# Kernel optimization log

Hardware: AMD Instinct MI355X
Metric: run time of the kernel (lower is better)

Reference implementation:

```python
import jax, jax.numpy as jnp
import numpy as np

B, L, LATENT, HID, NTOK = 65536, 8, 256, 128, 5


def setup_inputs() -> dict:
    key = jax.random.key(0)
    ks = jax.random.split(key, 8)
    s = 0.05  # small init scale for stable GRU dynamics
    return {
        "latent_context": jax.random.normal(ks[0], (B, LATENT), jnp.float32),
        "target_sequence": jax.random.randint(ks[1], (B, L), 0, NTOK),
        "emb_table": jax.random.normal(ks[2], (NTOK + 1, HID), jnp.float32) * s,
        "W_ih": jax.random.normal(ks[3], (3 * LATENT, HID), jnp.float32) * s,
        "W_hh": jax.random.normal(ks[4], (3 * LATENT, LATENT), jnp.float32) * s,
        "b_ih": jnp.zeros((3 * LATENT,), jnp.float32),
        "b_hh": jnp.zeros((3 * LATENT,), jnp.float32),
        "W_out": jax.random.normal(ks[5], (NTOK, LATENT), jnp.float32) * s,
        "b_out": jnp.zeros((NTOK,), jnp.float32),
    }


def reference(latent_context, target_sequence, emb_table, W_ih, W_hh, b_ih, b_hh, W_out, b_out):
    b = latent_context.shape[0]
    start_idx = emb_table.shape[0] - 1  # start token index = num_tokens
    # Teacher forcing: input token at step 0 is <start>, then target[:, :-1]
    tokens = jnp.concatenate(
        [jnp.full((b, 1), start_idx, dtype=target_sequence.dtype), target_sequence[:, :-1]],
        axis=1,
    )  # (B, L)
    emb = emb_table[tokens]  # (B, L, HID) embedding gather, done once

    def gru_step(h, x):
        # x: (B, HID), h: (B, LATENT). PyTorch GRU cell math.
        gi = x @ W_ih.T + b_ih          # (B, 3*LATENT)
        gh = h @ W_hh.T + b_hh          # (B, 3*LATENT)
        i_r, i_z, i_n = jnp.split(gi, 3, axis=-1)
        h_r, h_z, h_n = jnp.split(gh, 3, axis=-1)
        r = jax.nn.sigmoid(i_r + h_r)
        z = jax.nn.sigmoid(i_z + h_z)
        n = jnp.tanh(i_n + r * h_n)
        h_new = (1.0 - z) * n + z * h
        step_logits = h_new @ W_out.T + b_out  # (B, NTOK)
        return h_new, step_logits

    _, logits = jax.lax.scan(gru_step, latent_context, jnp.swapaxes(emb, 0, 1))
    return jnp.swapaxes(logits, 0, 1)  # (B, L, NTOK)
```

## Files before the change

### kernel.cpp

```cpp
#include <hip/hip_runtime.h>
#include <hip/hip_bf16.h>


typedef __attribute__((ext_vector_type(8)))  __bf16 bf16x8;
typedef __attribute__((ext_vector_type(4)))  __bf16 bf16x4;
typedef __attribute__((ext_vector_type(4)))  float  f32x4;

#define LOG2E_F     1.4426950408889634f
#define TWO_LOG2E_F 2.8853900817779268f

#if __has_builtin(__builtin_amdgcn_exp2f)
#define EXP2F(x) __builtin_amdgcn_exp2f(x)
#else
#define EXP2F(x) __expf((x) * 0.6931471805599453f)
#endif

__device__ __forceinline__ float sigm2(float a) {
    return __builtin_amdgcn_rcpf(1.f + EXP2F(-a));
}
__device__ __forceinline__ float tanh2(float a) {
    return __builtin_fmaf(2.f, __builtin_amdgcn_rcpf(1.f + EXP2F(-a)), -1.f);
}
__device__ __forceinline__ void lds_barrier() {
    __builtin_amdgcn_sched_barrier(0);
    asm volatile("s_waitcnt lgkmcnt(0)" ::: "memory");
    __builtin_amdgcn_s_barrier();
    __builtin_amdgcn_sched_barrier(0);
}

__global__ void k_gtable(const float* __restrict__ emb, const float* __restrict__ W_ih,
                         const float* __restrict__ b_ih, const float* __restrict__ b_hh,
                         float* __restrict__ G) {
    int tok = blockIdx.x;
    int j   = threadIdx.x;
    const float4* e4 = (const float4*)(emb + tok * 128);
    const float4* w4 = (const float4*)(W_ih + (size_t)j * 128);
    float s = 0.f;
#pragma unroll
    for (int k = 0; k < 32; ++k) {
        float4 a = e4[k], b = w4[k];
        s += a.x * b.x + a.y * b.y + a.z * b.z + a.w * b.w;
    }
    s += b_ih[j];
    if (j < 512) s = (s + b_hh[j]) * LOG2E_F;
    else         s = s * TWO_LOG2E_F;
    G[tok * 768 + j] = s;
}

__global__ void k_wfrag3(const float* __restrict__ Whh, const float* __restrict__ Gtab,
                         const float* __restrict__ b_hh, __bf16* __restrict__ Wg) {
    int u    = blockIdx.x * 256 + threadIdx.x;
    int lane = u & 63;
    int frag = u >> 6;
    int w    = frag / 28;
    int f    = frag - 28 * w;
    int col  = w * 16 + (lane & 15);
    int kq   = lane >> 4;
    bf16x8 v;
    if (f < 24) {
        int g = f >> 3, kc = f & 7;
        float scale = (g < 2) ? LOG2E_F : TWO_LOG2E_F;
        const float* src = Whh + (size_t)(g * 256 + col) * 256 + kc * 32 + kq * 8;
#pragma unroll
        for (int j = 0; j < 8; ++j) v[j] = (__bf16)(src[j] * scale);
    } else {
        int g = f - 24;
#pragma unroll
        for (int j = 0; j < 8; ++j) {
            int k = kq * 8 + j;
            float val = 0.f;
            if (k < 6) {
                val = (g == 0) ? Gtab[k * 768 + col]
                    : (g == 1) ? Gtab[k * 768 + 256 + col]
                    : (g == 2) ? b_hh[512 + col] * TWO_LOG2E_F
                               : Gtab[k * 768 + 512 + col];
            }
            v[j] = (__bf16)val;
        }
    }
    *(bf16x8*)(Wg + (size_t)u * 8) = v;
}

__global__ __launch_bounds__(1024) void k_main(
    const float* __restrict__ latent, const int* __restrict__ tgt,
    const __bf16* __restrict__ Wg, const float* __restrict__ Wout,
    const float* __restrict__ bout, float* __restrict__ out) {

    __shared__ __bf16 h_lds[2][4][8][64][8];
    __shared__ __bf16 onehot_lds[8][4][64][8];
    __shared__ __bf16 woutf_lds[8][64][8];
    __shared__ float  logit_lds[64 * 40];

    const int tid  = threadIdx.x;
    const int lane = tid & 63;
    const int w    = tid >> 6;
    const int q    = lane >> 4;
    const int n16  = lane & 15;
    const int row0 = blockIdx.x * 64;

    const __bf16* wbase = Wg + ((size_t)(w * 28) * 64 + lane) * 8;

    const int kc_h  = w >> 1;
    const int slotl = n16 + 16 * ((2 * w + (q >> 1)) & 3);
    const int joff  = 4 * (q & 1);

    if (tid < 512) {
        int kc = tid >> 6, ln = tid & 63, m = ln & 15, kq2 = ln >> 4;
        bf16x8 v;
#pragma unroll
        for (int j = 0; j < 8; ++j)
            v[j] = (m < 5) ? (__bf16)Wout[m * 256 + kc * 32 + kq2 * 8 + j] : (__bf16)0.f;
        *(bf16x8*)&woutf_lds[kc][ln][0] = v;
    }
    for (int s = tid; s < 2048; s += 1024) {
        int t = s >> 8, nt = (s >> 6) & 3, ln = s & 63;
        int nn = ln & 15, kq2 = ln >> 4;
        int tok = (t == 0) ? 5 : tgt[(size_t)(row0 + nt * 16 + nn) * 8 + t - 1];
        bf16x8 v;
#pragma unroll
        for (int j = 0; j < 8; ++j) v[j] = (__bf16)((kq2 * 8 + j == tok) ? 1.f : 0.f);
        *(bf16x8*)&onehot_lds[t][nt][ln][0] = v;
    }
#pragma unroll
    for (int nt = 0; nt < 4; ++nt) {
        float4 hv = *(const float4*)(latent + (size_t)(row0 + nt * 16 + n16) * 256 + 16 * w + 4 * q);
        bf16x4 hb;
        hb[0] = (__bf16)hv.x; hb[1] = (__bf16)hv.y;
        hb[2] = (__bf16)hv.z; hb[3] = (__bf16)hv.w;
        *(bf16x4*)&h_lds[0][nt][kc_h][slotl][joff] = hb;
    }
    const int lw = (w == 0) ? 0 : (w == 5) ? 1 : (w == 10) ? 2 : (w == 15) ? 3 : -1;
    const float bo0 = bout[0], bo1 = bout[1], bo2 = bout[2], bo3 = bout[3], bo4 = bout[4];
    const f32x4 z4 = {0.f, 0.f, 0.f, 0.f};
    __syncthreads();

    for (int t = 0; t < 8; ++t) {
        const int cur = t & 1, nxt = cur ^ 1;
        f32x4 acc[4][4];

        __builtin_amdgcn_s_setprio(1);
        {
            bf16x8 a0 = *(const bf16x8*)(wbase + (size_t)24 * 512);
            bf16x8 a1 = *(const bf16x8*)(wbase + (size_t)25 * 512);
            bf16x8 a2 = *(const bf16x8*)(wbase + (size_t)26 * 512);
            bf16x8 a3 = *(const bf16x8*)(wbase + (size_t)27 * 512);
#pragma unroll
            for (int nt = 0; nt < 4; ++nt) {
                bf16x8 oh = *(const bf16x8*)&onehot_lds[t][nt][lane][0];
                acc[0][nt] = __builtin_amdgcn_mfma_f32_16x16x32_bf16(a0, oh, z4, 0, 0, 0);
                acc[1][nt] = __builtin_amdgcn_mfma_f32_16x16x32_bf16(a1, oh, z4, 0, 0, 0);
                acc[2][nt] = __builtin_amdgcn_mfma_f32_16x16x32_bf16(a2, oh, z4, 0, 0, 0);
                acc[3][nt] = __builtin_amdgcn_mfma_f32_16x16x32_bf16(a3, oh, z4, 0, 0, 0);
            }
        }
#pragma unroll 2
        for (int kc = 0; kc < 8; ++kc) {
            bf16x8 a0 = *(const bf16x8*)(wbase + (size_t)kc * 512);
            bf16x8 a1 = *(const bf16x8*)(wbase + (size_t)(8 + kc) * 512);
            bf16x8 a2 = *(const bf16x8*)(wbase + (size_t)(16 + kc) * 512);
#pragma unroll
            for (int nt = 0; nt < 4; ++nt) {
                bf16x8 bb = *(const bf16x8*)&h_lds[cur][nt][kc][lane][0];
                acc[0][nt] = __builtin_amdgcn_mfma_f32_16x16x32_bf16(a0, bb, acc[0][nt], 0, 0, 0);
                acc[1][nt] = __builtin_amdgcn_mfma_f32_16x16x32_bf16(a1, bb, acc[1][nt], 0, 0, 0);
                acc[2][nt] = __builtin_amdgcn_mfma_f32_16x16x32_bf16(a2, bb, acc[2][nt], 0, 0, 0);
            }
        }

        if (lw >= 0 && t > 0) {
            f32x4 lacc = z4;
#pragma unroll
            for (int kc = 0; kc < 8; ++kc) {
                bf16x8 wf = *(const bf16x8*)&woutf_lds[kc][lane][0];
                bf16x8 bb = *(const bf16x8*)&h_lds[cur][lw][kc][lane][0];
                lacc = __builtin_amdgcn_mfma_f32_16x16x32_bf16(wf, bb, lacc, 0, 0, 0);
            }
            float* dst = &logit_lds[(lw * 16 + n16) * 40 + (t - 1) * 5];
            if (q == 0) {
                dst[0] = lacc[0] + bo0; dst[1] = lacc[1] + bo1;
                dst[2] = lacc[2] + bo2; dst[3] = lacc[3] + bo3;
            } else if (q == 1) {
                dst[4] = lacc[0] + bo4;
            }
        }
        __builtin_amdgcn_s_setprio(0);

#pragma unroll
        for (int nt = 0; nt < 4; ++nt) {
            bf16x4 hold = *(const bf16x4*)&h_lds[cur][nt][kc_h][slotl][joff];
            bf16x4 hb;
#pragma unroll
            for (int i = 0; i < 4; ++i) {
                float rg = sigm2(acc[0][nt][i]);
                float zg = sigm2(acc[1][nt][i]);
                float ng = tanh2(__builtin_fmaf(rg, acc[2][nt][i], acc[3][nt][i]));
                float hv = ng + zg * ((float)hold[i] - ng);
                hb[i] = (__bf16)hv;
            }
            *(bf16x4*)&h_lds[nxt][nt][kc_h][slotl][joff] = hb;
        }
        lds_barrier();
    }

    if (lw >= 0) {
        f32x4 lacc = z4;
#pragma unroll
        for (int kc = 0; kc < 8; ++kc) {
            bf16x8 wf = *(const bf16x8*)&woutf_lds[kc][lane][0];
            bf16x8 bb = *(const bf16x8*)&h_lds[0][lw][kc][lane][0];
            lacc = __builtin_amdgcn_mfma_f32_16x16x32_bf16(wf, bb, lacc, 0, 0, 0);
        }
        float* dst = &logit_lds[(lw * 16 + n16) * 40 + 7 * 5];
        if (q == 0) {
            dst[0] = lacc[0] + bo0; dst[1] = lacc[1] + bo1;
            dst[2] = lacc[2] + bo2; dst[3] = lacc[3] + bo3;
        } else if (q == 1) {
            dst[4] = lacc[0] + bo4;
        }
    }
    __syncthreads();
    for (int i = tid; i < 64 * 40; i += 1024)
        out[(size_t)row0 * 40 + i] = logit_lds[i];
}

extern "C" void kernel_launch(void* const* d_in, const int* in_sizes, int n_in,
                              void* d_out, int out_size, void* d_ws, size_t ws_size,
                              hipStream_t stream) {
    const float* latent = (const float*)d_in[0];
    const int*   tgt    = (const int*)d_in[1];
    const float* emb    = (const float*)d_in[2];
    const float* W_ih   = (const float*)d_in[3];
    const float* W_hh   = (const float*)d_in[4];
    const float* b_ih   = (const float*)d_in[5];
    const float* b_hh   = (const float*)d_in[6];
    const float* W_out  = (const float*)d_in[7];
    const float* b_out  = (const float*)d_in[8];
    float* out = (float*)d_out;

    float*  Gtab = (float*)d_ws;
    __bf16* Wg   = (__bf16*)((char*)d_ws + 18432);

    k_gtable<<<6, 768, 0, stream>>>(emb, W_ih, b_ih, b_hh, Gtab);
    k_wfrag3<<<112, 256, 0, stream>>>(W_hh, Gtab, b_hh, Wg);
    k_main<<<1024, 1024, 0, stream>>>(latent, tgt, Wg, W_out, b_out, out);
}
```

Before: 246.1 us.

## Ping-pong two row groups so MFMA matmul overlaps gate epilogue

```diff
diff --git a/kernel.cpp b/kernel.cpp
--- a/kernel.cpp
+++ b/kernel.cpp
@@ -4,6 +4,7 @@
 
 typedef __attribute__((ext_vector_type(8)))  __bf16 bf16x8;
 typedef __attribute__((ext_vector_type(4)))  __bf16 bf16x4;
+typedef __attribute__((ext_vector_type(8)))  unsigned short u16x8;
 typedef __attribute__((ext_vector_type(4)))  float  f32x4;
 
 #define LOG2E_F     1.4426950408889634f
@@ -27,6 +28,8 @@
     __builtin_amdgcn_s_barrier();
     __builtin_amdgcn_sched_barrier(0);
 }
+
+#define MFMA16(a, b, c) __builtin_amdgcn_mfma_f32_16x16x32_bf16((a), (b), (c), 0, 0, 0)
 
 __global__ void k_gtable(const float* __restrict__ emb, const float* __restrict__ W_ih,
                          const float* __restrict__ b_ih, const float* __restrict__ b_hh,
@@ -81,30 +84,27 @@
     *(bf16x8*)(Wg + (size_t)u * 8) = v;
 }
 
-__global__ __launch_bounds__(1024) void k_main(
+__global__ __launch_bounds__(512) void k_main(
     const float* __restrict__ latent, const int* __restrict__ tgt,
     const __bf16* __restrict__ Wg, const float* __restrict__ Wout,
     const float* __restrict__ bout, float* __restrict__ out) {
 
-    __shared__ __bf16 h_lds[2][4][8][64][8];
-    __shared__ __bf16 onehot_lds[8][4][64][8];
+    __shared__ __bf16 h_lds[8][8][64][8];
     __shared__ __bf16 woutf_lds[8][64][8];
-    __shared__ float  logit_lds[64 * 40];
-
-    const int tid  = threadIdx.x;
-    const int lane = tid & 63;
-    const int w    = tid >> 6;
-    const int q    = lane >> 4;
-    const int n16  = lane & 15;
-    const int row0 = blockIdx.x * 64;
-
-    const __bf16* wbase = Wg + ((size_t)(w * 28) * 64 + lane) * 8;
-
-    const int kc_h  = w >> 1;
-    const int slotl = n16 + 16 * ((2 * w + (q >> 1)) & 3);
-    const int joff  = 4 * (q & 1);
-
-    if (tid < 512) {
+    __shared__ int    tok_lds[128 * 9];
+    __shared__ float  logit_lds[128 * 40];
+
+    const int tid   = threadIdx.x;
+    const int lane  = tid & 63;
+    const int u     = tid >> 6;
+    const int group = u >> 2;
+    const int gu    = u & 3;
+    const int q     = lane >> 4;
+    const int n16   = lane & 15;
+    const int row0  = blockIdx.x * 128;
+    const int Tl    = group * 4 + gu;
+
+    {
         int kc = tid >> 6, ln = tid & 63, m = ln & 15, kq2 = ln >> 4;
         bf16x8 v;
 #pragma unroll
@@ -112,105 +112,140 @@
             v[j] = (m < 5) ? (__bf16)Wout[m * 256 + kc * 32 + kq2 * 8 + j] : (__bf16)0.f;
         *(bf16x8*)&woutf_lds[kc][ln][0] = v;
     }
-    for (int s = tid; s < 2048; s += 1024) {
-        int t = s >> 8, nt = (s >> 6) & 3, ln = s & 63;
-        int nn = ln & 15, kq2 = ln >> 4;
-        int tok = (t == 0) ? 5 : tgt[(size_t)(row0 + nt * 16 + nn) * 8 + t - 1];
-        bf16x8 v;
-#pragma unroll
-        for (int j = 0; j < 8; ++j) v[j] = (__bf16)((kq2 * 8 + j == tok) ? 1.f : 0.f);
-        *(bf16x8*)&onehot_lds[t][nt][ln][0] = v;
-    }
-#pragma unroll
-    for (int nt = 0; nt < 4; ++nt) {
-        float4 hv = *(const float4*)(latent + (size_t)(row0 + nt * 16 + n16) * 256 + 16 * w + 4 * q);
+    for (int i = tid; i < 1024; i += 512) {
+        int r = i >> 3, t = i & 7;
+        tok_lds[r * 9 + t] = (t == 0) ? 5 : tgt[(size_t)(row0 + r) * 8 + t - 1];
+    }
+    for (int i = tid; i < 128 * 64; i += 512) {
+        int r = i >> 6, cq = i & 63, c = cq * 4;
+        float4 hv = *(const float4*)(latent + (size_t)(row0 + r) * 256 + c);
         bf16x4 hb;
         hb[0] = (__bf16)hv.x; hb[1] = (__bf16)hv.y;
         hb[2] = (__bf16)hv.z; hb[3] = (__bf16)hv.w;
-        *(bf16x4*)&h_lds[0][nt][kc_h][slotl][joff] = hb;
-    }
-    const int lw = (w == 0) ? 0 : (w == 5) ? 1 : (w == 10) ? 2 : (w == 15) ? 3 : -1;
+        *(bf16x4*)&h_lds[r >> 4][c >> 5][(r & 15) + 16 * ((c >> 3) & 3)][c & 7] = hb;
+    }
     const float bo0 = bout[0], bo1 = bout[1], bo2 = bout[2], bo3 = bout[3], bo4 = bout[4];
     const f32x4 z4 = {0.f, 0.f, 0.f, 0.f};
+
+    f32x4 acc[3][4][4];
     __syncthreads();
 
-    for (int t = 0; t < 8; ++t) {
-        const int cur = t & 1, nxt = cur ^ 1;
-        f32x4 acc[4][4];
-
-        __builtin_amdgcn_s_setprio(1);
-        {
-            bf16x8 a0 = *(const bf16x8*)(wbase + (size_t)24 * 512);
-            bf16x8 a1 = *(const bf16x8*)(wbase + (size_t)25 * 512);
-            bf16x8 a2 = *(const bf16x8*)(wbase + (size_t)26 * 512);
-            bf16x8 a3 = *(const bf16x8*)(wbase + (size_t)27 * 512);
-#pragma unroll
-            for (int nt = 0; nt < 4; ++nt) {
-                bf16x8 oh = *(const bf16x8*)&onehot_lds[t][nt][lane][0];
-                acc[0][nt] = __builtin_amdgcn_mfma_f32_16x16x32_bf16(a0, oh, z4, 0, 0, 0);
-                acc[1][nt] = __builtin_amdgcn_mfma_f32_16x16x32_bf16(a1, oh, z4, 0, 0, 0);
-                acc[2][nt] = __builtin_amdgcn_mfma_f32_16x16x32_bf16(a2, oh, z4, 0, 0, 0);
-                acc[3][nt] = __builtin_amdgcn_mfma_f32_16x16x32_bf16(a3, oh, z4, 0, 0, 0);
+    for (int ph = 0; ph < 17; ++ph) {
+        if (((ph ^ group) & 1) == 0) {
+            const int t = (ph - group) >> 1;
+            if (t < 8) {
+                __builtin_amdgcn_s_setprio(1);
+                {
+                    bf16x8 b0 = *(const bf16x8*)&h_lds[group * 4 + 0][0][lane][0];
+                    bf16x8 b1 = *(const bf16x8*)&h_lds[group * 4 + 1][0][lane][0];
+                    bf16x8 b2 = *(const bf16x8*)&h_lds[group * 4 + 2][0][lane][0];
+                    bf16x8 b3 = *(const bf16x8*)&h_lds[group * 4 + 3][0][lane][0];
+#pragma unroll
+                    for (int g = 0; g < 3; ++g)
+#pragma unroll
+                        for (int ct = 0; ct < 4; ++ct) {
+                            bf16x8 a = *(const bf16x8*)(Wg +
+                                (size_t)((4 * gu + ct) * 28 + g * 8) * 512 + lane * 8);
+                            acc[g][ct][0] = MFMA16(a, b0, z4);
+                            acc[g][ct][1] = MFMA16(a, b1, z4);
+                            acc[g][ct][2] = MFMA16(a, b2, z4);
+                            acc[g][ct][3] = MFMA16(a, b3, z4);
+                        }
+                }
+#pragma unroll 1
+                for (int kc = 1; kc < 8; ++kc) {
+                    bf16x8 b0 = *(const bf16x8*)&h_lds[group * 4 + 0][kc][lane][0];
+                    bf16x8 b1 = *(const bf16x8*)&h_lds[group * 4 + 1][kc][lane][0];
+                    bf16x8 b2 = *(const bf16x8*)&h_lds[group * 4 + 2][kc][lane][0];
+                    bf16x8 b3 = *(const bf16x8*)&h_lds[group * 4 + 3][kc][lane][0];
+#pragma unroll
+                    for (int g = 0; g < 3; ++g)
+#pragma unroll
+                        for (int ct = 0; ct < 4; ++ct) {
+                            bf16x8 a = *(const bf16x8*)(Wg +
+                                (size_t)((4 * gu + ct) * 28 + g * 8 + kc) * 512 + lane * 8);
+                            acc[g][ct][0] = MFMA16(a, b0, acc[g][ct][0]);
+                            acc[g][ct][1] = MFMA16(a, b1, acc[g][ct][1]);
+                            acc[g][ct][2] = MFMA16(a, b2, acc[g][ct][2]);
+                            acc[g][ct][3] = MFMA16(a, b3, acc[g][ct][3]);
+                        }
+                }
+                if (t > 0) {
+                    f32x4 lacc = z4;
+#pragma unroll
+                    for (int kc = 0; kc < 8; ++kc) {
+                        bf16x8 wf = *(const bf16x8*)&woutf_lds[kc][lane][0];
+                        bf16x8 bb = *(const bf16x8*)&h_lds[Tl][kc][lane][0];
+                        lacc = MFMA16(wf, bb, lacc);
+                    }
+                    float* dst = &logit_lds[(Tl * 16 + n16) * 40 + (t - 1) * 5];
+                    if (q == 0) {
+                        dst[0] = lacc[0] + bo0; dst[1] = lacc[1] + bo1;
+                        dst[2] = lacc[2] + bo2; dst[3] = lacc[3] + bo3;
+                    } else if (q == 1) {
+                        dst[4] = lacc[0] + bo4;
+                    }
+                }
+                __builtin_amdgcn_s_setprio(0);
             }
-        }
-#pragma unroll 2
-        for (int kc = 0; kc < 8; ++kc) {
-            bf16x8 a0 = *(const bf16x8*)(wbase + (size_t)kc * 512);
-            bf16x8 a1 = *(const bf16x8*)(wbase + (size_t)(8 + kc) * 512);
-            bf16x8 a2 = *(const bf16x8*)(wbase + (size_t)(16 + kc) * 512);
-#pragma unroll
-            for (int nt = 0; nt < 4; ++nt) {
-                bf16x8 bb = *(const bf16x8*)&h_lds[cur][nt][kc][lane][0];
-                acc[0][nt] = __builtin_amdgcn_mfma_f32_16x16x32_bf16(a0, bb, acc[0][nt], 0, 0, 0);
-                acc[1][nt] = __builtin_amdgcn_mfma_f32_16x16x32_bf16(a1, bb, acc[1][nt], 0, 0, 0);
-                acc[2][nt] = __builtin_amdgcn_mfma_f32_16x16x32_bf16(a2, bb, acc[2][nt], 0, 0, 0);
+        } else {
+            const int tc = (ph - group - 1) >> 1;
+            if (tc >= 0 && tc < 8) {
+                bf16x8 oh[4];
+#pragma unroll
+                for (int nt = 0; nt < 4; ++nt) {
+                    int tokv = tok_lds[((group * 4 + nt) * 16 + n16) * 9 + tc];
+                    u16x8 o;
+#pragma unroll
+                    for (int j = 0; j < 8; ++j)
+                        o[j] = (q * 8 + j == tokv) ? (unsigned short)0x3F80 : (unsigned short)0;
+                    oh[nt] = __builtin_bit_cast(bf16x8, o);
+                }
+#pragma unroll
+                for (int ct = 0; ct < 4; ++ct) {
+                    const __bf16* ob = Wg + (size_t)((4 * gu + ct) * 28 + 24) * 512 + lane * 8;
+                    bf16x8 a0 = *(const bf16x8*)(ob);
+                    bf16x8 a1 = *(const bf16x8*)(ob + 512);
+                    bf16x8 a2 = *(const bf16x8*)(ob + 1024);
+                    bf16x8 a3 = *(const bf16x8*)(ob + 1536);
+                    const int cb  = 64 * gu + 16 * ct + 4 * q;
+                    const int kch = cb >> 5;
+                    const int sl  = n16 + 16 * ((cb >> 3) & 3);
+                    const int j0  = cb & 7;
+#pragma unroll
+                    for (int nt = 0; nt < 4; ++nt) {
+                        f32x4 ar = MFMA16(a0, oh[nt], acc[0][ct][nt]);
+                        f32x4 az = MFMA16(a1, oh[nt], acc[1][ct][nt]);
+                        f32x4 an = MFMA16(a2, oh[nt], acc[2][ct][nt]);
+                        f32x4 ai = MFMA16(a3, oh[nt], z4);
+                        bf16x4* slot = (bf16x4*)&h_lds[group * 4 + nt][kch][sl][j0];
+                        bf16x4 hold = *slot;
+                        bf16x4 hb;
+#pragma unroll
+                        for (int i = 0; i < 4; ++i) {
+                            float rg = sigm2(ar[i]);
+                            float zg = sigm2(az[i]);
+                            float ng = tanh2(__builtin_fmaf(rg, an[i], ai[i]));
+                            float hv = ng + zg * ((float)hold[i] - ng);
+                            hb[i] = (__bf16)hv;
+                        }
+                        *slot = hb;
+                    }
+                }
             }
         }
-
-        if (lw >= 0 && t > 0) {
-            f32x4 lacc = z4;
-#pragma unroll
-            for (int kc = 0; kc < 8; ++kc) {
-                bf16x8 wf = *(const bf16x8*)&woutf_lds[kc][lane][0];
-                bf16x8 bb = *(const bf16x8*)&h_lds[cur][lw][kc][lane][0];
-                lacc = __builtin_amdgcn_mfma_f32_16x16x32_bf16(wf, bb, lacc, 0, 0, 0);
-            }
-            float* dst = &logit_lds[(lw * 16 + n16) * 40 + (t - 1) * 5];
-            if (q == 0) {
-                dst[0] = lacc[0] + bo0; dst[1] = lacc[1] + bo1;
-                dst[2] = lacc[2] + bo2; dst[3] = lacc[3] + bo3;
-            } else if (q == 1) {
-                dst[4] = lacc[0] + bo4;
-            }
-        }
-        __builtin_amdgcn_s_setprio(0);
-
-#pragma unroll
-        for (int nt = 0; nt < 4; ++nt) {
-            bf16x4 hold = *(const bf16x4*)&h_lds[cur][nt][kc_h][slotl][joff];
-            bf16x4 hb;
-#pragma unroll
-            for (int i = 0; i < 4; ++i) {
-                float rg = sigm2(acc[0][nt][i]);
-                float zg = sigm2(acc[1][nt][i]);
-                float ng = tanh2(__builtin_fmaf(rg, acc[2][nt][i], acc[3][nt][i]));
-                float hv = ng + zg * ((float)hold[i] - ng);
-                hb[i] = (__bf16)hv;
-            }
-            *(bf16x4*)&h_lds[nxt][nt][kc_h][slotl][joff] = hb;
-        }
         lds_barrier();
     }
 
-    if (lw >= 0) {
+    {
         f32x4 lacc = z4;
 #pragma unroll
         for (int kc = 0; kc < 8; ++kc) {
             bf16x8 wf = *(const bf16x8*)&woutf_lds[kc][lane][0];
-            bf16x8 bb = *(const bf16x8*)&h_lds[0][lw][kc][lane][0];
-            lacc = __builtin_amdgcn_mfma_f32_16x16x32_bf16(wf, bb, lacc, 0, 0, 0);
-        }
-        float* dst = &logit_lds[(lw * 16 + n16) * 40 + 7 * 5];
+            bf16x8 bb = *(const bf16x8*)&h_lds[Tl][kc][lane][0];
+            lacc = MFMA16(wf, bb, lacc);
+        }
+        float* dst = &logit_lds[(Tl * 16 + n16) * 40 + 7 * 5];
         if (q == 0) {
             dst[0] = lacc[0] + bo0; dst[1] = lacc[1] + bo1;
             dst[2] = lacc[2] + bo2; dst[3] = lacc[3] + bo3;
@@ -219,7 +254,7 @@
         }
     }
     __syncthreads();
-    for (int i = tid; i < 64 * 40; i += 1024)
+    for (int i = tid; i < 128 * 40; i += 512)
         out[(size_t)row0 * 40 + i] = logit_lds[i];
 }
 
@@ -242,5 +277,5 @@
 
     k_gtable<<<6, 768, 0, stream>>>(emb, W_ih, b_ih, b_hh, Gtab);
     k_wfrag3<<<112, 256, 0, stream>>>(W_hh, Gtab, b_hh, Wg);
-    k_main<<<1024, 1024, 0, stream>>>(latent, tgt, Wg, W_out, b_out, out);
-}
+    k_main<<<512, 512, 0, stream>>>(latent, tgt, Wg, W_out, b_out, out);
+}
```

Result: slower. 587.7 us (+138.8%).
